# Kernel tuning notes

Measured on AMD Instinct MI355X. Metric: run time of the kernel, lower is better.

The kernel has to match this reference:

```python
import jax, jax.numpy as jnp
import numpy as np

HEADS1, HID1 = 4, 64   # layer 1: concat -> 256
HEADS2, HID2 = 1, 64   # layer 2: out_channels
NEG_SLOPE = 0.2


def gat_layer(x_src, x_dst, W_src, W_dst, att_src, att_dst, bias, src, dst, n_tgt, heads, hid):
    # bipartite GATConv (PyG math), concat heads
    xs = (x_src @ W_src).reshape(-1, heads, hid)          # [Ns,H,C]
    xd = (x_dst @ W_dst).reshape(-1, heads, hid)          # [Nt,H,C]
    a_s = jnp.sum(xs * att_src, axis=-1)                  # [Ns,H]
    a_d = jnp.sum(xd * att_dst, axis=-1)                  # [Nt,H]
    e = jax.nn.leaky_relu(a_s[src] + a_d[dst], NEG_SLOPE) # [E,H]
    m = jax.ops.segment_max(e, dst, num_segments=n_tgt)
    m = jnp.where(jnp.isfinite(m), m, 0.0)
    ex = jnp.exp(e - m[dst])
    denom = jax.ops.segment_sum(ex, dst, num_segments=n_tgt)
    alpha = ex / (denom[dst] + 1e-16)                     # edge softmax per target
    msg = xs[src] * alpha[:, :, None]                     # [E,H,C]
    out = jax.ops.segment_sum(msg, dst, num_segments=n_tgt)
    return out.reshape(n_tgt, heads * hid) + bias


def setup_inputs() -> dict:
    key = jax.random.key(0)
    ks = jax.random.split(key, 20)
    N0, NT1, NT2 = 100000, 25000, 5000
    E1, E2 = 400000, 100000
    IN, H1 = 256, HEADS1 * HID1  # 256
    OUT = HEADS2 * HID2          # 64
    g = lambda k, sh, fan: jax.random.normal(k, sh, jnp.float32) * (1.0 / np.sqrt(fan))
    return {
        'x': jax.random.normal(ks[0], (N0, IN), jnp.float32),
        'src1': jax.random.randint(ks[1], (E1,), 0, N0),
        'dst1': jax.random.randint(ks[2], (E1,), 0, NT1),
        'src2': jax.random.randint(ks[3], (E2,), 0, NT1),
        'dst2': jax.random.randint(ks[4], (E2,), 0, NT2),
        'n_tgt1': NT1, 'n_tgt2': NT2,
        'W1_src': g(ks[5], (IN, H1), IN), 'W1_dst': g(ks[6], (IN, H1), IN),
        'att1_src': g(ks[7], (HEADS1, HID1), HID1), 'att1_dst': g(ks[8], (HEADS1, HID1), HID1),
        'bias1': jnp.zeros((H1,), jnp.float32),
        'skip1_W': g(ks[9], (IN, H1), IN), 'skip1_b': jnp.zeros((H1,), jnp.float32),
        'W2_src': g(ks[10], (H1, OUT), H1), 'W2_dst': g(ks[11], (H1, OUT), H1),
        'att2_src': g(ks[12], (HEADS2, HID2), HID2), 'att2_dst': g(ks[13], (HEADS2, HID2), HID2),
        'bias2': jnp.zeros((OUT,), jnp.float32),
        'skip2_W': g(ks[14], (H1, OUT), H1), 'skip2_b': jnp.zeros((OUT,), jnp.float32),
    }


def reference(x, src1, dst1, src2, dst2, n_tgt1, n_tgt2,
              W1_src, W1_dst, att1_src, att1_dst, bias1, skip1_W, skip1_b,
              W2_src, W2_dst, att2_src, att2_dst, bias2, skip2_W, skip2_b):
    # layer 1: conv + skip + elu (dropout inactive in eval)
    x_t1 = x[:n_tgt1]
    h = gat_layer(x, x_t1, W1_src, W1_dst, att1_src, att1_dst, bias1,
                  src1, dst1, n_tgt1, HEADS1, HID1)
    h = h + (x_t1 @ skip1_W + skip1_b)
    h = jax.nn.elu(h)
    # layer 2 (final): conv + skip, then log_softmax
    x_t2 = h[:n_tgt2]
    o = gat_layer(h, x_t2, W2_src, W2_dst, att2_src, att2_dst, bias2,
                  src2, dst2, n_tgt2, HEADS2, HID2)
    o = o + (x_t2 @ skip2_W + skip2_b)
    return jax.nn.log_softmax(o, axis=-1)
```

## Files before the change

### kernel.cpp

```cpp
#include <hip/hip_runtime.h>
#include <hip/hip_bf16.h>

using bf16 = __hip_bfloat16;
typedef __attribute__((ext_vector_type(8))) short short8;
typedef __attribute__((ext_vector_type(4))) short short4v;
typedef __attribute__((ext_vector_type(4))) float float4v;

__device__ __forceinline__ short f2bs(float x) {
    bf16 b = __float2bfloat16(x);
    return __builtin_bit_cast(short, b);
}
__device__ __forceinline__ float bs2f(short s) {
    return __uint_as_float(((unsigned)(unsigned short)s) << 16);
}
__device__ __forceinline__ void glds16(const void* g, void* l) {
    __builtin_amdgcn_global_load_lds(
        (const __attribute__((address_space(1))) unsigned int*)g,
        (__attribute__((address_space(3))) unsigned int*)l, 16, 0, 0);
}

__global__ __launch_bounds__(256, 2) void gemm_l1(
        const float* __restrict__ A, const bf16* __restrict__ Bt,
        bf16* __restrict__ xs1, bf16* __restrict__ sk1,
        float* __restrict__ as1, float* __restrict__ ad1,
        const float* __restrict__ att_s, const float* __restrict__ att_d,
        int M, int NT) {
    __shared__ short ldsB[2][16 * 512];
    const int row0 = blockIdx.x * 128;
    const int tid = threadIdx.x;
    const int wave = tid >> 6, lane = tid & 63;
    const int quad = lane >> 4, l16 = lane & 15;
    const int ymax = row0 < NT ? 12 : 4;
    const int Hmax = 2 * ymax;

    auto stageH = [&](int H, int buf) {
#pragma unroll
        for (int i = 0; i < 4; i++) {
            int blk = wave * 4 + i;
            int cb = blk >> 3, kit = blk & 7;
            glds16(&Bt[(size_t)(H * 32 + cb * 16 + l16) * 256 + kit * 32 + quad * 8],
                   &ldsB[buf][blk * 512]);
        }
    };
    stageH(0, 0);

    short8 afr[2][8];
    {
        int r0_ = row0 + wave * 32 + l16;
        int r1_ = r0_ + 16;
        const int ra = r0_ < M ? r0_ : M - 1;
        const int rb = r1_ < M ? r1_ : M - 1;
        const float* Ap0 = &A[(size_t)ra * 256 + quad * 8];
        const float* Ap1 = &A[(size_t)rb * 256 + quad * 8];
#pragma unroll
        for (int m = 0; m < 2; m++) {
            const float* Apm = m == 0 ? Ap0 : Ap1;
#pragma unroll
            for (int half = 0; half < 2; half++) {
                float4v r0[4], r1[4];
#pragma unroll
                for (int k = 0; k < 4; k++) {
                    const float* p = Apm + (half * 4 + k) * 32;
                    r0[k] = *(const float4v*)(p);
                    r1[k] = *(const float4v*)(p + 4);
                }
#pragma unroll
                for (int k = 0; k < 4; k++) {
                    short8 v;
#pragma unroll
                    for (int j = 0; j < 4; j++) {
                        v[j] = f2bs(r0[k][j]); v[4 + j] = f2bs(r1[k][j]);
                    }
                    afr[m][half * 4 + k] = v;
                }
            }
        }
    }

    const int rbase = row0 + wave * 32 + quad * 4;
    __syncthreads();

    float4v acc[2][4];
    for (int H = 0; H < Hmax; H++) {
        const int buf = H & 1;
        if (H + 1 < Hmax) stageH(H + 1, buf ^ 1);

        if ((H & 1) == 0) {
            const float4v fz = {0.f, 0.f, 0.f, 0.f};
#pragma unroll
            for (int m = 0; m < 2; m++)
#pragma unroll
                for (int n = 0; n < 4; n++) acc[m][n] = fz;
#pragma unroll
            for (int kit = 0; kit < 8; kit++)
#pragma unroll
                for (int nf = 0; nf < 2; nf++) {
                    short8 bf = *(short8*)&ldsB[buf][(nf * 8 + kit) * 512 + lane * 8];
#pragma unroll
                    for (int m = 0; m < 2; m++)
                        acc[m][nf] = __builtin_amdgcn_mfma_f32_16x16x32_bf16(
                            afr[m][kit], bf, acc[m][nf], 0, 0, 0);
                }
        } else {
#pragma unroll
            for (int kit = 0; kit < 8; kit++)
#pragma unroll
                for (int nf = 0; nf < 2; nf++) {
                    short8 bf = *(short8*)&ldsB[buf][(nf * 8 + kit) * 512 + lane * 8];
#pragma unroll
                    for (int m = 0; m < 2; m++)
                        acc[m][2 + nf] = __builtin_amdgcn_mfma_f32_16x16x32_bf16(
                            afr[m][kit], bf, acc[m][2 + nf], 0, 0, 0);
                }

            const int y = H >> 1;
            if (y < 8) {
                const float* attc = y < 4 ? att_s : att_d;
                const int head = y & 3;
                const int aM = y < 4 ? M : NT;
                float* aout = y < 4 ? as1 : ad1;
                float av[4];
#pragma unroll
                for (int n = 0; n < 4; n++) av[n] = attc[head * 64 + n * 16 + l16];
#pragma unroll
                for (int m = 0; m < 2; m++)
#pragma unroll
                    for (int r = 0; r < 4; r++) {
                        float t = acc[m][0][r] * av[0] + acc[m][1][r] * av[1] +
                                  acc[m][2][r] * av[2] + acc[m][3][r] * av[3];
                        t += __shfl_xor(t, 1, 64);
                        t += __shfl_xor(t, 2, 64);
                        t += __shfl_xor(t, 4, 64);
                        t += __shfl_xor(t, 8, 64);
                        int grow = rbase + m * 16 + r;
                        if (l16 == 0 && grow < aM) aout[(size_t)grow * 4 + head] = t;
                    }
            }
            if (y < 4) {
#pragma unroll
                for (int m = 0; m < 2; m++)
#pragma unroll
                    for (int n = 0; n < 4; n++) {
                        int col = y * 64 + n * 16 + l16;
#pragma unroll
                        for (int r = 0; r < 4; r++) {
                            int row = rbase + m * 16 + r;
                            if (row < M)
                                xs1[(size_t)row * 256 + col] = __float2bfloat16(acc[m][n][r]);
                        }
                    }
            } else if (y >= 8) {
#pragma unroll
                for (int m = 0; m < 2; m++)
#pragma unroll
                    for (int n = 0; n < 4; n++) {
                        int scol = (y - 8) * 64 + n * 16 + l16;
#pragma unroll
                        for (int r = 0; r < 4; r++) {
                            int row = rbase + m * 16 + r;
                            if (row < NT)
                                sk1[(size_t)row * 256 + scol] = __float2bfloat16(acc[m][n][r]);
                        }
                    }
            }
        }
        __syncthreads();
    }
}

__global__ __launch_bounds__(512, 4) void gemm_l2(
        const bf16* __restrict__ Ah, const bf16* __restrict__ Bt,
        float* __restrict__ x2, float* __restrict__ a2,
        const float* __restrict__ attc, int NT) {
    __shared__ short ldsB[32 * 512];
    const int y = blockIdx.y;
    const int row0 = blockIdx.x * 128;
    const int col0 = y * 64;
    const int tid = threadIdx.x;
    const int wave = tid >> 6, lane = tid & 63;
    const int quad = lane >> 4, l16 = lane & 15;

#pragma unroll
    for (int i = 0; i < 4; i++) {
        int blk = wave * 4 + i;
        int cb = blk >> 3, kit = blk & 7;
        glds16(&Bt[(size_t)(col0 + cb * 16 + l16) * 256 + kit * 32 + quad * 8],
               &ldsB[blk * 512]);
    }

    const int arow = row0 + wave * 16 + l16;
    const bf16* Ap = &Ah[(size_t)arow * 256 + quad * 8];

    short8 s[8];
#pragma unroll
    for (int kit = 0; kit < 8; kit++) s[kit] = *(const short8*)(Ap + kit * 32);

    const float4v fz = {0.f, 0.f, 0.f, 0.f};
    float4v acc[4];
#pragma unroll
    for (int n = 0; n < 4; n++) acc[n] = fz;

    __syncthreads();

#pragma unroll
    for (int kit = 0; kit < 8; kit++) {
#pragma unroll
        for (int n = 0; n < 4; n++) {
            short8 bf = *(short8*)&ldsB[(n * 8 + kit) * 512 + lane * 8];
            acc[n] = __builtin_amdgcn_mfma_f32_16x16x32_bf16(s[kit], bf, acc[n], 0, 0, 0);
        }
    }

    const int rbase = row0 + wave * 16 + quad * 4;

    if (y < 2) {
        float av[4];
#pragma unroll
        for (int n = 0; n < 4; n++) av[n] = attc[y * 64 + n * 16 + l16];
#pragma unroll
        for (int r = 0; r < 4; r++) {
            float t = acc[0][r] * av[0] + acc[1][r] * av[1] +
                      acc[2][r] * av[2] + acc[3][r] * av[3];
            t += __shfl_xor(t, 1, 64);
            t += __shfl_xor(t, 2, 64);
            t += __shfl_xor(t, 4, 64);
            t += __shfl_xor(t, 8, 64);
            int grow = rbase + r;
            if (l16 == 0 && grow < NT) a2[(size_t)grow * 2 + y] = t;
        }
    }
#pragma unroll
    for (int n = 0; n < 4; n++) {
        int col = col0 + n * 16 + l16;
#pragma unroll
        for (int r = 0; r < 4; r++) {
            int row = rbase + r;
            if (row < NT) x2[(size_t)row * 192 + col] = acc[n][r];
        }
    }
}

__global__ void prep_s(
        const int* __restrict__ s1, const int* __restrict__ d1, int E1,
        const int* __restrict__ s2, const int* __restrict__ d2, int E2,
        int* __restrict__ fill1, int* __restrict__ fill2,
        int* __restrict__ psrc1, int* __restrict__ psrc2,
        const float* __restrict__ W1s, const float* __restrict__ W1d,
        const float* __restrict__ W1sk, const float* __restrict__ W2s,
        const float* __restrict__ W2d, const float* __restrict__ W2sk,
        const float* __restrict__ a2s, const float* __restrict__ a2d,
        bf16* __restrict__ Wt1, bf16* __restrict__ Wt2,
        float* __restrict__ at2c) {
    int t = blockIdx.x * blockDim.x + threadIdx.x;
    if (t < E1) {
        int d = d1[t];
        int pos = atomicAdd(&fill1[d], 1);
        if (pos < 64) psrc1[(d << 6) + pos] = s1[t];
        return;
    }
    t -= E1;
    if (t < E2) {
        int d = d2[t];
        int pos = atomicAdd(&fill2[d], 1);
        if (pos < 64) psrc2[(d << 6) + pos] = s2[t];
        return;
    }
    t -= E2;
    if (t < 196608) {
        int n = t >> 8, k = t & 255;
        const float* W = n < 256 ? W1s : (n < 512 ? W1d : W1sk);
        Wt1[t] = __float2bfloat16(W[k * 256 + (n & 255)]);
    } else if (t < 245760) {
        int i = t - 196608;
        int n = i >> 8, k = i & 255;
        const float* W = n < 64 ? W2s : (n < 128 ? W2d : W2sk);
        Wt2[i] = __float2bfloat16(W[k * 64 + (n & 63)]);
    } else if (t < 245888) {
        int i = t - 245760;
        at2c[i] = i < 64 ? a2s[i] : a2d[i - 64];
    }
}

__global__ __launch_bounds__(256) void agg_h4(
        const int* __restrict__ fill, const int* __restrict__ psrc,
        const bf16* __restrict__ X, const float* __restrict__ as1,
        const float* __restrict__ ad1, const float* __restrict__ bias,
        const bf16* __restrict__ skip, const float* __restrict__ skipb,
        bf16* __restrict__ h) {
    __shared__ float exl[4][64][4];
    __shared__ float red[4][256];
    const int d = blockIdx.x;
    const int tid = threadIdx.x;
    const int wv = tid >> 6, lane = tid & 63;
    const int head = lane >> 4;
    int deg = fill[d];
    deg = deg < 64 ? deg : 64;
    int se = 0;
    float4v ex4 = {0.f, 0.f, 0.f, 0.f};
    const float4v ad4 = *(const float4v*)&ad1[(size_t)d * 4];
    if (lane < deg) {
        se = psrc[((size_t)d << 6) + lane];
        float4v as4 = *(const float4v*)&as1[(size_t)se * 4];
#pragma unroll
        for (int c = 0; c < 4; c++) {
            float v = as4[c] + ad4[c];
            v = v > 0.f ? v : 0.2f * v;
            ex4[c] = expf(v);
        }
    }
    *(float4v*)&exl[wv][lane][0] = ex4;
    float4v dn = ex4;
#pragma unroll
    for (int o = 32; o; o >>= 1) {
        dn.x += __shfl_xor(dn.x, o, 64);
        dn.y += __shfl_xor(dn.y, o, 64);
        dn.z += __shfl_xor(dn.z, o, 64);
        dn.w += __shfl_xor(dn.w, o, 64);
    }
    float4v acc = {0.f, 0.f, 0.f, 0.f}, acc2 = {0.f, 0.f, 0.f, 0.f};
    int p = wv;
    for (; p + 4 < deg; p += 8) {
        int sA = __shfl(se, p, 64), sB = __shfl(se, p + 4, 64);
        float aA = exl[wv][p][head], aB = exl[wv][p + 4][head];
        short4v xa = *(const short4v*)&X[(size_t)sA * 256 + lane * 4];
        short4v xb = *(const short4v*)&X[(size_t)sB * 256 + lane * 4];
        acc.x += bs2f(xa.x) * aA; acc2.x += bs2f(xb.x) * aB;
        acc.y += bs2f(xa.y) * aA; acc2.y += bs2f(xb.y) * aB;
        acc.z += bs2f(xa.z) * aA; acc2.z += bs2f(xb.z) * aB;
        acc.w += bs2f(xa.w) * aA; acc2.w += bs2f(xb.w) * aB;
    }
    for (; p < deg; p += 4) {
        int sA = __shfl(se, p, 64);
        float aA = exl[wv][p][head];
        short4v xa = *(const short4v*)&X[(size_t)sA * 256 + lane * 4];
        acc.x += bs2f(xa.x) * aA;
        acc.y += bs2f(xa.y) * aA;
        acc.z += bs2f(xa.z) * aA;
        acc.w += bs2f(xa.w) * aA;
    }
    acc.x += acc2.x; acc.y += acc2.y; acc.z += acc2.z; acc.w += acc2.w;
    *(float4v*)&red[wv][lane * 4] = acc;
    __syncthreads();
    const int f = tid;
    float sum = red[0][f] + red[1][f] + red[2][f] + red[3][f];
    int hf = f >> 6;
    float den = hf == 0 ? dn.x : hf == 1 ? dn.y : hf == 2 ? dn.z : dn.w;
    float v = sum / (den + 1e-16f) + bias[f] + __bfloat162float(skip[(size_t)d * 256 + f]) +
              skipb[f];
    h[(size_t)d * 256 + f] = __float2bfloat16(v > 0.f ? v : expm1f(v));
}

__global__ __launch_bounds__(256) void agg_h1(
        const int* __restrict__ fill2, const int* __restrict__ psrc2,
        const float* __restrict__ x2, const float* __restrict__ a2,
        const float* __restrict__ bias, const float* __restrict__ skipb,
        float* __restrict__ out, int M) {
    const int d = blockIdx.x * 4 + (threadIdx.x >> 6);
    const int lane = threadIdx.x & 63;
    if (d >= M) return;
    int deg = fill2[d];
    deg = deg < 64 ? deg : 64;
    int se = 0;
    float exv = 0.f;
    const float adv = a2[(size_t)d * 2 + 1];
    if (lane < deg) {
        se = psrc2[((size_t)d << 6) + lane];
        float v = a2[(size_t)se * 2] + adv;
        v = v > 0.f ? v : 0.2f * v;
        exv = expf(v);
    }
    float den = exv;
#pragma unroll
    for (int o = 32; o; o >>= 1) den += __shfl_xor(den, o, 64);
    float acc = 0.f, acc2 = 0.f;
    int p = 0;
    for (; p + 1 < deg; p += 2) {
        int sA = __shfl(se, p, 64), sB = __shfl(se, p + 1, 64);
        float aA = __shfl(exv, p, 64), aB = __shfl(exv, p + 1, 64);
        acc += x2[(size_t)sA * 192 + lane] * aA;
        acc2 += x2[(size_t)sB * 192 + lane] * aB;
    }
    if (p < deg) {
        int sA = __shfl(se, p, 64);
        acc += x2[(size_t)sA * 192 + lane] * __shfl(exv, p, 64);
    }
    float v = (acc + acc2) / (den + 1e-16f) + bias[lane] +
              x2[(size_t)d * 192 + 128 + lane] + skipb[lane];
    float m = v;
#pragma unroll
    for (int o = 32; o; o >>= 1) m = fmaxf(m, __shfl_xor(m, o, 64));
    float e = expf(v - m);
#pragma unroll
    for (int o = 32; o; o >>= 1) e += __shfl_xor(e, o, 64);
    out[(size_t)d * 64 + lane] = v - m - logf(e);
}

extern "C" void kernel_launch(void* const* d_in, const int* in_sizes, int n_in,
                              void* d_out, int out_size, void* d_ws, size_t ws_size,
                              hipStream_t stream) {
    const float* x        = (const float*)d_in[0];
    const int*   src1     = (const int*)d_in[1];
    const int*   dst1     = (const int*)d_in[2];
    const int*   src2     = (const int*)d_in[3];
    const int*   dst2     = (const int*)d_in[4];
    const float* W1_src   = (const float*)d_in[7];
    const float* W1_dst   = (const float*)d_in[8];
    const float* att1_src = (const float*)d_in[9];
    const float* att1_dst = (const float*)d_in[10];
    const float* bias1    = (const float*)d_in[11];
    const float* skip1_W  = (const float*)d_in[12];
    const float* skip1_b  = (const float*)d_in[13];
    const float* W2_src   = (const float*)d_in[14];
    const float* W2_dst   = (const float*)d_in[15];
    const float* att2_src = (const float*)d_in[16];
    const float* att2_dst = (const float*)d_in[17];
    const float* bias2    = (const float*)d_in[18];
    const float* skip2_W  = (const float*)d_in[19];
    const float* skip2_b  = (const float*)d_in[20];

    const int N0  = in_sizes[0] / 256;
    const int E1  = in_sizes[1];
    const int E2  = in_sizes[3];
    const int NT1 = 25000, NT2 = 5000;
    const int NT1p = 25088;

    char* ws = (char*)d_ws;
    size_t off = 0;
    auto alloc = [&](size_t b) { size_t o = off; off += (b + 255) & ~(size_t)255; return o; };
    size_t o_xs1   = alloc((size_t)N0 * 256 * 2);
    size_t o_sk1   = alloc((size_t)NT1 * 256 * 2);
    size_t o_h     = alloc((size_t)NT1p * 256 * 2);
    size_t o_as1   = alloc((size_t)N0 * 4 * 4);
    size_t o_ad1   = alloc((size_t)NT1 * 4 * 4);
    size_t o_fill  = alloc((size_t)(NT1 + NT2) * 4);
    size_t o_psrc1 = alloc((size_t)NT1 * 64 * 4);
    size_t o_psrc2 = alloc((size_t)NT2 * 64 * 4);
    size_t o_wt1   = alloc((size_t)768 * 256 * 2);
    size_t o_wt2   = alloc((size_t)192 * 256 * 2);
    size_t o_at2c  = alloc((size_t)128 * 4);
    size_t off2a = o_xs1;
    auto alloc2 = [&](size_t b) { size_t o = off2a; off2a += (b + 255) & ~(size_t)255; return o; };
    size_t o_x2 = alloc2((size_t)NT1 * 192 * 4);
    size_t o_a2 = alloc2((size_t)NT1 * 2 * 4);

    bf16*  xs1   = (bf16*)(ws + o_xs1);
    bf16*  sk1   = (bf16*)(ws + o_sk1);
    bf16*  h     = (bf16*)(ws + o_h);
    float* as1   = (float*)(ws + o_as1);
    float* ad1   = (float*)(ws + o_ad1);
    int*   fill1 = (int*)(ws + o_fill);
    int*   fill2 = fill1 + NT1;
    int*   psrc1 = (int*)(ws + o_psrc1);
    int*   psrc2 = (int*)(ws + o_psrc2);
    bf16*  Wt1   = (bf16*)(ws + o_wt1);
    bf16*  Wt2   = (bf16*)(ws + o_wt2);
    float* at2c  = (float*)(ws + o_at2c);
    float* x2    = (float*)(ws + o_x2);
    float* a2    = (float*)(ws + o_a2);

    hipMemsetAsync(fill1, 0, (size_t)(NT1 + NT2) * 4, stream);
    {
        int total = E1 + E2 + 245888;
        prep_s<<<(total + 255) / 256, 256, 0, stream>>>(
            src1, dst1, E1, src2, dst2, E2, fill1, fill2, psrc1, psrc2,
            W1_src, W1_dst, skip1_W, W2_src, W2_dst, skip2_W,
            att2_src, att2_dst, Wt1, Wt2, at2c);
    }
    gemm_l1<<<(N0 + 127) / 128, 256, 0, stream>>>(
        x, Wt1, xs1, sk1, as1, ad1, att1_src, att1_dst, N0, NT1);
    agg_h4<<<NT1, 256, 0, stream>>>(fill1, psrc1, xs1, as1, ad1, bias1, sk1, skip1_b, h);
    gemm_l2<<<dim3((NT1 + 127) / 128, 3), 512, 0, stream>>>(h, Wt2, x2, a2, at2c, NT1);
    agg_h1<<<(NT2 + 3) / 4, 256, 0, stream>>>(fill2, psrc2, x2, a2, bias2, skip2_b,
                                              (float*)d_out, NT2);
}
```

Baseline: 328.6 us.

## Map one wavefront per target node in layer-1 aggregation

The layer-1 aggregation kernel now processes four target nodes per block, one wavefront each, instead of one node per block split across four wavefronts. This removes the shared-memory cross-wave reduction and the block barrier. The epilogue now reads skip values and writes output as 4-wide vectors. In exchange, each wavefront walks every edge of its node alone, which cuts memory-level parallelism per node from two loads in flight per wave to two per node. Average degree is about 16, so per-node latency becomes longer.

```diff
diff --git a/kernel.cpp b/kernel.cpp
--- a/kernel.cpp
+++ b/kernel.cpp
@@ -286,12 +286,11 @@
         const bf16* __restrict__ X, const float* __restrict__ as1,
         const float* __restrict__ ad1, const float* __restrict__ bias,
         const bf16* __restrict__ skip, const float* __restrict__ skipb,
-        bf16* __restrict__ h) {
+        bf16* __restrict__ h, int M) {
     __shared__ float exl[4][64][4];
-    __shared__ float red[4][256];
-    const int d = blockIdx.x;
-    const int tid = threadIdx.x;
-    const int wv = tid >> 6, lane = tid & 63;
+    const int wv = threadIdx.x >> 6, lane = threadIdx.x & 63;
+    const int d = blockIdx.x * 4 + wv;
+    if (d >= M) return;
     const int head = lane >> 4;
     int deg = fill[d];
     deg = deg < 64 ? deg : 64;
@@ -318,10 +317,10 @@
         dn.w += __shfl_xor(dn.w, o, 64);
     }
     float4v acc = {0.f, 0.f, 0.f, 0.f}, acc2 = {0.f, 0.f, 0.f, 0.f};
-    int p = wv;
-    for (; p + 4 < deg; p += 8) {
-        int sA = __shfl(se, p, 64), sB = __shfl(se, p + 4, 64);
-        float aA = exl[wv][p][head], aB = exl[wv][p + 4][head];
+    int p = 0;
+    for (; p + 1 < deg; p += 2) {
+        int sA = __shfl(se, p, 64), sB = __shfl(se, p + 1, 64);
+        float aA = exl[wv][p][head], aB = exl[wv][p + 1][head];
         short4v xa = *(const short4v*)&X[(size_t)sA * 256 + lane * 4];
         short4v xb = *(const short4v*)&X[(size_t)sB * 256 + lane * 4];
         acc.x += bs2f(xa.x) * aA; acc2.x += bs2f(xb.x) * aB;
@@ -329,7 +328,7 @@
         acc.z += bs2f(xa.z) * aA; acc2.z += bs2f(xb.z) * aB;
         acc.w += bs2f(xa.w) * aA; acc2.w += bs2f(xb.w) * aB;
     }
-    for (; p < deg; p += 4) {
+    if (p < deg) {
         int sA = __shfl(se, p, 64);
         float aA = exl[wv][p][head];
         short4v xa = *(const short4v*)&X[(size_t)sA * 256 + lane * 4];
@@ -339,15 +338,24 @@
         acc.w += bs2f(xa.w) * aA;
     }
     acc.x += acc2.x; acc.y += acc2.y; acc.z += acc2.z; acc.w += acc2.w;
-    *(float4v*)&red[wv][lane * 4] = acc;
-    __syncthreads();
-    const int f = tid;
-    float sum = red[0][f] + red[1][f] + red[2][f] + red[3][f];
-    int hf = f >> 6;
-    float den = hf == 0 ? dn.x : hf == 1 ? dn.y : hf == 2 ? dn.z : dn.w;
-    float v = sum / (den + 1e-16f) + bias[f] + __bfloat162float(skip[(size_t)d * 256 + f]) +
-              skipb[f];
-    h[(size_t)d * 256 + f] = __float2bfloat16(v > 0.f ? v : expm1f(v));
+    const int f0 = lane * 4;
+    float den = head == 0 ? dn.x : head == 1 ? dn.y : head == 2 ? dn.z : dn.w;
+    den += 1e-16f;
+    short4v sk = *(const short4v*)&skip[(size_t)d * 256 + f0];
+    float4v bi = *(const float4v*)&bias[f0];
+    float4v sb = *(const float4v*)&skipb[f0];
+    short4v out;
+    {
+        float v0 = acc.x / den + bi.x + bs2f(sk.x) + sb.x;
+        float v1 = acc.y / den + bi.y + bs2f(sk.y) + sb.y;
+        float v2 = acc.z / den + bi.z + bs2f(sk.z) + sb.z;
+        float v3 = acc.w / den + bi.w + bs2f(sk.w) + sb.w;
+        out.x = f2bs(v0 > 0.f ? v0 : expm1f(v0));
+        out.y = f2bs(v1 > 0.f ? v1 : expm1f(v1));
+        out.z = f2bs(v2 > 0.f ? v2 : expm1f(v2));
+        out.w = f2bs(v3 > 0.f ? v3 : expm1f(v3));
+    }
+    *(short4v*)&h[(size_t)d * 256 + f0] = out;
 }
 
 __global__ __launch_bounds__(256) void agg_h1(
@@ -468,7 +476,8 @@
     }
     gemm_l1<<<(N0 + 127) / 128, 256, 0, stream>>>(
         x, Wt1, xs1, sk1, as1, ad1, att1_src, att1_dst, N0, NT1);
-    agg_h4<<<NT1, 256, 0, stream>>>(fill1, psrc1, xs1, as1, ad1, bias1, sk1, skip1_b, h);
+    agg_h4<<<(NT1 + 3) / 4, 256, 0, stream>>>(fill1, psrc1, xs1, as1, ad1, bias1,
+                                              sk1, skip1_b, h, NT1);
     gemm_l2<<<dim3((NT1 + 127) / 128, 3), 512, 0, stream>>>(h, Wt2, x2, a2, at2c, NT1);
     agg_h1<<<(NT2 + 3) / 4, 256, 0, stream>>>(fill2, psrc2, x2, a2, bias2, skip2_b,
                                               (float*)d_out, NT2);
```

Result: faster. 316.7 us (-3.6%).
